# Kernel optimization log

Hardware: AMD Instinct MI355X
Metric: run time of the kernel (lower is better)

Reference implementation:

```python
import jax, jax.numpy as jnp
import numpy as np

N = 50000   # nodes
E = 800000  # edges (avg degree 16)
F_IN, F_HID, F_OUT = 4, 64, 1


def setup_inputs() -> dict:
    key = jax.random.key(0)
    k1, k2, k3, k4 = jax.random.split(key, 4)
    x = jax.random.normal(k1, (N, F_IN), dtype=jnp.float32)
    edge_index = jax.random.randint(k2, (2, E), 0, N, dtype=jnp.int64)
    W1 = jax.random.normal(k3, (F_IN, F_HID), dtype=jnp.float32) * (1.0 / np.sqrt(F_IN))
    b1 = jnp.zeros((F_HID,), dtype=jnp.float32)
    W2 = jax.random.normal(k4, (F_HID, F_OUT), dtype=jnp.float32) * (1.0 / np.sqrt(F_HID))
    b2 = jnp.zeros((F_OUT,), dtype=jnp.float32)
    return {"x": x, "edge_index": edge_index, "W1": W1, "b1": b1, "W2": W2, "b2": b2}


def _gcn_conv(h, W, b, src, dst, norm, n_nodes):
    # h: [N, F_in] -> linear -> gather src -> scale by norm -> scatter-add at dst
    m = (h @ W)[src] * norm[:, None]          # [E+N, F_out]
    out = jax.ops.segment_sum(m, dst, num_segments=n_nodes)
    return out + b


def reference(x, edge_index, W1, b1, W2, b2):
    n = x.shape[0]
    loops = jnp.arange(n, dtype=edge_index.dtype)
    src = jnp.concatenate([edge_index[0], loops])  # add self loops (PyG default)
    dst = jnp.concatenate([edge_index[1], loops])
    # symmetric normalization: deg computed at target (col) as in PyG gcn_norm
    deg = jax.ops.segment_sum(jnp.ones_like(dst, dtype=x.dtype), dst, num_segments=n)
    dis = jnp.where(deg > 0, deg ** -0.5, 0.0)
    norm = dis[src] * dis[dst]                      # [E+N]

    h = jax.nn.relu(_gcn_conv(x, W1, b1, src, dst, norm, n))
    # F.dropout with training=False (inference) is identity
    out = _gcn_conv(h, W2, b2, src, dst, norm, n)
    return jax.nn.sigmoid(out)                      # [N, 1]
```

## Files before the change

kernel.cpp:

```cpp
#include <hip/hip_runtime.h>
#include <hip/hip_fp16.h>


#define FH 64
#define NPB 256
#define MAXBK 512
#define CHB 2048
#define BCAP 8192

__global__ void k_bkt_fill(const int* __restrict__ src, const int* __restrict__ dst,
                           int* __restrict__ bcnt, unsigned int* __restrict__ ebuf,
                           int E, int nbk) {
    __shared__ int h[MAXBK];
    __shared__ int resv[MAXBK];
    int t = threadIdx.x;
    for (int i = t; i < nbk; i += 256) h[i] = 0;
    __syncthreads();
    int base = blockIdx.x * CHB;
    int end = min(base + CHB, E);
    for (int e = base + t; e < end; e += 256)
        atomicAdd(&h[dst[e] >> 8], 1);
    __syncthreads();
    for (int i = t; i < nbk; i += 256) {
        int c = h[i];
        resv[i] = c ? atomicAdd(&bcnt[i], c) : 0;
        h[i] = 0;
    }
    __syncthreads();
    for (int e = base + t; e < end; e += 256) {
        int d = dst[e];
        int b = d >> 8;
        int idx = resv[b] + atomicAdd(&h[b], 1);
        if (idx < BCAP)
            ebuf[(size_t)b * BCAP + idx] = ((unsigned int)d << 16) | (unsigned int)src[e];
    }
}

__global__ void k_bkt_finish(const unsigned int* __restrict__ ebuf,
                             const int* __restrict__ bcnt,
                             int* __restrict__ rowptr, float* __restrict__ dis,
                             unsigned short* __restrict__ csr, int N) {
    __shared__ int sc[NPB];
    __shared__ int f[NPB];
    __shared__ int sbase;
    int b = blockIdx.x, t = threadIdx.x;
    int s = 0;
    for (int i = t; i < b; i += 256) s += bcnt[i];
    sc[t] = s;
    __syncthreads();
    for (int off = 128; off; off >>= 1) {
        if (t < off) sc[t] += sc[t + off];
        __syncthreads();
    }
    if (t == 0) sbase = sc[0];
    __syncthreads();
    int ebase = sbase;
    int cnt = min(bcnt[b], BCAP);
    const unsigned int* eb = ebuf + (size_t)b * BCAP;
    f[t] = 0;
    __syncthreads();
    for (int j = t; j < cnt; j += 256)
        atomicAdd(&f[(eb[j] >> 16) & (NPB - 1)], 1);
    __syncthreads();
    int myc = f[t];
    sc[t] = myc;
    __syncthreads();
    for (int off = 1; off < NPB; off <<= 1) {
        int add = (t >= off) ? sc[t - off] : 0;
        __syncthreads();
        sc[t] += add;
        __syncthreads();
    }
    int ex = ebase + sc[t] - myc;
    int node = b * NPB + t;
    if (node < N) {
        rowptr[node] = ex;
        dis[node] = rsqrtf((float)(myc + 1));
    }
    if (node == N - 1) rowptr[N] = ex + myc;
    __syncthreads();
    f[t] = ex;
    __syncthreads();
    for (int j = t; j < cnt; j += 256) {
        unsigned int pe = eb[j];
        int p = atomicAdd(&f[(pe >> 16) & (NPB - 1)], 1);
        csr[p] = (unsigned short)(pe & 0xffffu);
    }
}

__global__ void k_lin1(const float* __restrict__ x, const float* __restrict__ W1,
                       const float* __restrict__ dis, __half* __restrict__ g, int n) {
    __shared__ float sW[4 * FH];
    int t = threadIdx.x;
    sW[t] = W1[t];
    __syncthreads();
    int node = blockIdx.x * 4 + (t >> 6);
    int f = t & 63;
    if (node < n) {
        float4 xv = *reinterpret_cast<const float4*>(x + (size_t)node * 4);
        float v = xv.x * sW[f] + xv.y * sW[FH + f] + xv.z * sW[2 * FH + f] + xv.w * sW[3 * FH + f];
        g[(size_t)node * FH + f] = __float2half_rn(v * dis[node]);
    }
}

__global__ void k_layer1(const int* __restrict__ rowptr, const unsigned short* __restrict__ csr,
                         const __half* __restrict__ g, const float* __restrict__ dis,
                         const float* __restrict__ b1, const float* __restrict__ W2,
                         float* __restrict__ q, int n) {
    int t = threadIdx.x;
    int node = blockIdx.x * 4 + (t >> 6);
    int f = t & 63;
    if (node >= n) return;
    int rs = rowptr[node], re = rowptr[node + 1];
    float acc = __half2float(g[(size_t)node * FH + f]);
    int j = rs;
    for (; j + 3 < re; j += 4) {
        int s0 = csr[j], s1 = csr[j + 1], s2 = csr[j + 2], s3 = csr[j + 3];
        acc += __half2float(g[(size_t)s0 * FH + f]);
        acc += __half2float(g[(size_t)s1 * FH + f]);
        acc += __half2float(g[(size_t)s2 * FH + f]);
        acc += __half2float(g[(size_t)s3 * FH + f]);
    }
    for (; j < re; ++j) acc += __half2float(g[(size_t)csr[j] * FH + f]);
    float dn = dis[node];
    float h = fmaxf(dn * acc + b1[f], 0.0f);
    float v = h * W2[f];
    #pragma unroll
    for (int off = 32; off; off >>= 1) v += __shfl_xor(v, off, 64);
    if (f == 0) q[node] = v * dn;
}

__global__ void k_layer2(const int* __restrict__ rowptr, const unsigned short* __restrict__ csr,
                         const float* __restrict__ q, const float* __restrict__ dis,
                         const float* __restrict__ b2, float* __restrict__ out, int n) {
    int i = blockIdx.x * blockDim.x + threadIdx.x;
    if (i >= n) return;
    int rs = rowptr[i], re = rowptr[i + 1];
    float acc = q[i];
    for (int j = rs; j < re; ++j) acc += q[csr[j]];
    float v = dis[i] * acc + b2[0];
    out[i] = 1.0f / (1.0f + __expf(-v));
}

extern "C" void kernel_launch(void* const* d_in, const int* in_sizes, int n_in,
                              void* d_out, int out_size, void* d_ws, size_t ws_size,
                              hipStream_t stream) {
    const float* x   = (const float*)d_in[0];
    const int*   ei  = (const int*)d_in[1];
    const float* W1  = (const float*)d_in[2];
    const float* b1  = (const float*)d_in[3];
    const float* W2  = (const float*)d_in[4];
    const float* b2  = (const float*)d_in[5];
    float* out = (float*)d_out;

    int N = in_sizes[0] / 4;
    int E = in_sizes[1] / 2;
    const int* src = ei;
    const int* dst = ei + E;
    int nbk = (N + NPB - 1) / NPB;
    int nbe = (E + CHB - 1) / CHB;

    char* ws = (char*)d_ws;
    size_t off = 0;
    auto alloc = [&](size_t bytes) {
        void* p = ws + off;
        off = (off + bytes + 255) & ~(size_t)255;
        return p;
    };
    int*            rowptr = (int*)alloc((size_t)(N + 1) * 4);
    float*          dis    = (float*)alloc((size_t)N * 4);
    unsigned short* csr    = (unsigned short*)alloc((size_t)E * 2);
    __half*         g      = (__half*)alloc((size_t)N * FH * 2);
    float*          q      = (float*)alloc((size_t)N * 4);
    int*            bcnt   = (int*)alloc((size_t)MAXBK * 4);
    unsigned int*   ebuf   = (unsigned int*)alloc((size_t)nbk * BCAP * 4);
    (void)ws_size;

    hipMemsetAsync(bcnt, 0, (size_t)MAXBK * 4, stream);

    k_bkt_fill<<<nbe, 256, 0, stream>>>(src, dst, bcnt, ebuf, E, nbk);
    k_bkt_finish<<<nbk, 256, 0, stream>>>(ebuf, bcnt, rowptr, dis, csr, N);

    k_lin1<<<(N + 3) / 4, 256, 0, stream>>>(x, W1, dis, g, N);
    k_layer1<<<(N + 3) / 4, 256, 0, stream>>>(rowptr, csr, g, dis, b1, W2, q, N);
    k_layer2<<<(N + 255) / 256, 256, 0, stream>>>(rowptr, csr, q, dis, b2, out, N);
}
```

Measured before the change: 151.3 us.

## Fuse all GCN stages into one cooperative persistent kernel with grid syncs

Replaces the five separate kernel launches with a single cooperative kernel that runs the bucket fill, CSR finish, linear layer, layer-1 aggregation and layer-2 aggregation in sequence, separated by grid-wide barriers. The linear transform no longer depends on the degree normalization, so it is folded into the bucket-fill phase, and the per-source normalization is applied during aggregation instead. The aim is to cut launch and inter-kernel gap overhead. In exchange the aggregation does an extra gather of dis per edge, the grid is fixed at 1024 blocks, and the grid.sync barriers add their own cost.

```diff
diff --git a/kernel.cpp b/kernel.cpp
--- a/kernel.cpp
+++ b/kernel.cpp
@@ -1,5 +1,8 @@
 #include <hip/hip_runtime.h>
 #include <hip/hip_fp16.h>
+#include <hip/hip_cooperative_groups.h>
+
+namespace cg = cooperative_groups;
 
 
 #define FH 64
@@ -7,139 +10,155 @@
 #define MAXBK 512
 #define CHB 2048
 #define BCAP 8192
-
-__global__ void k_bkt_fill(const int* __restrict__ src, const int* __restrict__ dst,
-                           int* __restrict__ bcnt, unsigned int* __restrict__ ebuf,
-                           int E, int nbk) {
+#define GRID_BLKS 1024
+
+struct Params {
+    const int* src; const int* dst;
+    const float* x; const float* W1; const float* b1; const float* W2; const float* b2;
+    float* out;
+    int* rowptr; float* dis; unsigned short* csr; __half* g; float* q;
+    int* bcnt; unsigned int* ebuf;
+    int N, E, nbk, nbe, npass;
+};
+
+__global__ void __launch_bounds__(256) k_mega(Params p) {
+    cg::grid_group grid = cg::this_grid();
+    const int t = threadIdx.x;
+    const int bid = blockIdx.x;
+    const int nb = gridDim.x;
+
     __shared__ int h[MAXBK];
     __shared__ int resv[MAXBK];
-    int t = threadIdx.x;
-    for (int i = t; i < nbk; i += 256) h[i] = 0;
+    __shared__ int sc[NPB];
+    __shared__ int ff[NPB];
+    __shared__ float sW[4 * FH];
+    __shared__ int sbase;
+
+    sW[t] = p.W1[t];
     __syncthreads();
-    int base = blockIdx.x * CHB;
-    int end = min(base + CHB, E);
-    for (int e = base + t; e < end; e += 256)
-        atomicAdd(&h[dst[e] >> 8], 1);
-    __syncthreads();
-    for (int i = t; i < nbk; i += 256) {
-        int c = h[i];
-        resv[i] = c ? atomicAdd(&bcnt[i], c) : 0;
-        h[i] = 0;
-    }
-    __syncthreads();
-    for (int e = base + t; e < end; e += 256) {
-        int d = dst[e];
-        int b = d >> 8;
-        int idx = resv[b] + atomicAdd(&h[b], 1);
-        if (idx < BCAP)
-            ebuf[(size_t)b * BCAP + idx] = ((unsigned int)d << 16) | (unsigned int)src[e];
-    }
-}
-
-__global__ void k_bkt_finish(const unsigned int* __restrict__ ebuf,
-                             const int* __restrict__ bcnt,
-                             int* __restrict__ rowptr, float* __restrict__ dis,
-                             unsigned short* __restrict__ csr, int N) {
-    __shared__ int sc[NPB];
-    __shared__ int f[NPB];
-    __shared__ int sbase;
-    int b = blockIdx.x, t = threadIdx.x;
-    int s = 0;
-    for (int i = t; i < b; i += 256) s += bcnt[i];
-    sc[t] = s;
-    __syncthreads();
-    for (int off = 128; off; off >>= 1) {
-        if (t < off) sc[t] += sc[t + off];
-        __syncthreads();
-    }
-    if (t == 0) sbase = sc[0];
-    __syncthreads();
-    int ebase = sbase;
-    int cnt = min(bcnt[b], BCAP);
-    const unsigned int* eb = ebuf + (size_t)b * BCAP;
-    f[t] = 0;
-    __syncthreads();
-    for (int j = t; j < cnt; j += 256)
-        atomicAdd(&f[(eb[j] >> 16) & (NPB - 1)], 1);
-    __syncthreads();
-    int myc = f[t];
-    sc[t] = myc;
-    __syncthreads();
-    for (int off = 1; off < NPB; off <<= 1) {
-        int add = (t >= off) ? sc[t - off] : 0;
-        __syncthreads();
-        sc[t] += add;
-        __syncthreads();
-    }
-    int ex = ebase + sc[t] - myc;
-    int node = b * NPB + t;
-    if (node < N) {
-        rowptr[node] = ex;
-        dis[node] = rsqrtf((float)(myc + 1));
-    }
-    if (node == N - 1) rowptr[N] = ex + myc;
-    __syncthreads();
-    f[t] = ex;
-    __syncthreads();
-    for (int j = t; j < cnt; j += 256) {
-        unsigned int pe = eb[j];
-        int p = atomicAdd(&f[(pe >> 16) & (NPB - 1)], 1);
-        csr[p] = (unsigned short)(pe & 0xffffu);
-    }
-}
-
-__global__ void k_lin1(const float* __restrict__ x, const float* __restrict__ W1,
-                       const float* __restrict__ dis, __half* __restrict__ g, int n) {
-    __shared__ float sW[4 * FH];
-    int t = threadIdx.x;
-    sW[t] = W1[t];
-    __syncthreads();
-    int node = blockIdx.x * 4 + (t >> 6);
-    int f = t & 63;
-    if (node < n) {
-        float4 xv = *reinterpret_cast<const float4*>(x + (size_t)node * 4);
-        float v = xv.x * sW[f] + xv.y * sW[FH + f] + xv.z * sW[2 * FH + f] + xv.w * sW[3 * FH + f];
-        g[(size_t)node * FH + f] = __float2half_rn(v * dis[node]);
-    }
-}
-
-__global__ void k_layer1(const int* __restrict__ rowptr, const unsigned short* __restrict__ csr,
-                         const __half* __restrict__ g, const float* __restrict__ dis,
-                         const float* __restrict__ b1, const float* __restrict__ W2,
-                         float* __restrict__ q, int n) {
-    int t = threadIdx.x;
-    int node = blockIdx.x * 4 + (t >> 6);
-    int f = t & 63;
-    if (node >= n) return;
-    int rs = rowptr[node], re = rowptr[node + 1];
-    float acc = __half2float(g[(size_t)node * FH + f]);
-    int j = rs;
-    for (; j + 3 < re; j += 4) {
-        int s0 = csr[j], s1 = csr[j + 1], s2 = csr[j + 2], s3 = csr[j + 3];
-        acc += __half2float(g[(size_t)s0 * FH + f]);
-        acc += __half2float(g[(size_t)s1 * FH + f]);
-        acc += __half2float(g[(size_t)s2 * FH + f]);
-        acc += __half2float(g[(size_t)s3 * FH + f]);
-    }
-    for (; j < re; ++j) acc += __half2float(g[(size_t)csr[j] * FH + f]);
-    float dn = dis[node];
-    float h = fmaxf(dn * acc + b1[f], 0.0f);
-    float v = h * W2[f];
-    #pragma unroll
-    for (int off = 32; off; off >>= 1) v += __shfl_xor(v, off, 64);
-    if (f == 0) q[node] = v * dn;
-}
-
-__global__ void k_layer2(const int* __restrict__ rowptr, const unsigned short* __restrict__ csr,
-                         const float* __restrict__ q, const float* __restrict__ dis,
-                         const float* __restrict__ b2, float* __restrict__ out, int n) {
-    int i = blockIdx.x * blockDim.x + threadIdx.x;
-    if (i >= n) return;
-    int rs = rowptr[i], re = rowptr[i + 1];
-    float acc = q[i];
-    for (int j = rs; j < re; ++j) acc += q[csr[j]];
-    float v = dis[i] * acc + b2[0];
-    out[i] = 1.0f / (1.0f + __expf(-v));
+
+    for (int c = bid; c < p.nbe; c += nb) {
+        for (int i = t; i < p.nbk; i += 256) h[i] = 0;
+        __syncthreads();
+        int base = c * CHB, end = min(base + CHB, p.E);
+        for (int e = base + t; e < end; e += 256)
+            atomicAdd(&h[p.dst[e] >> 8], 1);
+        __syncthreads();
+        for (int i = t; i < p.nbk; i += 256) {
+            int cc = h[i];
+            resv[i] = cc ? atomicAdd(&p.bcnt[i], cc) : 0;
+            h[i] = 0;
+        }
+        __syncthreads();
+        for (int e = base + t; e < end; e += 256) {
+            int d = p.dst[e];
+            int b = d >> 8;
+            int idx = resv[b] + atomicAdd(&h[b], 1);
+            if (idx < BCAP)
+                p.ebuf[(size_t)b * BCAP + idx] = ((unsigned)d << 16) | (unsigned)p.src[e];
+        }
+        __syncthreads();
+    }
+
+    for (int pass = bid; pass < p.npass; pass += nb) {
+        int node = pass * 4 + (t >> 6), f = t & 63;
+        if (node < p.N) {
+            float4 xv = *reinterpret_cast<const float4*>(p.x + (size_t)node * 4);
+            float v = xv.x * sW[f] + xv.y * sW[FH + f] + xv.z * sW[2 * FH + f] + xv.w * sW[3 * FH + f];
+            p.g[(size_t)node * FH + f] = __float2half_rn(v);
+        }
+    }
+
+    grid.sync();
+
+    for (int b = bid; b < p.nbk; b += nb) {
+        int s = 0;
+        for (int i = t; i < b; i += 256) s += p.bcnt[i];
+        sc[t] = s;
+        __syncthreads();
+        for (int off = 128; off; off >>= 1) {
+            if (t < off) sc[t] += sc[t + off];
+            __syncthreads();
+        }
+        if (t == 0) sbase = sc[0];
+        __syncthreads();
+        int ebase = sbase;
+        int cnt = min(p.bcnt[b], BCAP);
+        const unsigned int* eb = p.ebuf + (size_t)b * BCAP;
+        ff[t] = 0;
+        __syncthreads();
+        for (int j = t; j < cnt; j += 256)
+            atomicAdd(&ff[(eb[j] >> 16) & (NPB - 1)], 1);
+        __syncthreads();
+        int myc = ff[t];
+        sc[t] = myc;
+        __syncthreads();
+        for (int off = 1; off < NPB; off <<= 1) {
+            int add = (t >= off) ? sc[t - off] : 0;
+            __syncthreads();
+            sc[t] += add;
+            __syncthreads();
+        }
+        int ex = ebase + sc[t] - myc;
+        int node = b * NPB + t;
+        if (node < p.N) {
+            p.rowptr[node] = ex;
+            p.dis[node] = rsqrtf((float)(myc + 1));
+        }
+        if (node == p.N - 1) p.rowptr[p.N] = ex + myc;
+        __syncthreads();
+        ff[t] = ex;
+        __syncthreads();
+        for (int j = t; j < cnt; j += 256) {
+            unsigned int pe = eb[j];
+            int pos = atomicAdd(&ff[(pe >> 16) & (NPB - 1)], 1);
+            p.csr[pos] = (unsigned short)(pe & 0xffffu);
+        }
+        __syncthreads();
+    }
+
+    grid.sync();
+
+    {
+        int f = t & 63;
+        int w = (bid << 2) + (t >> 6);
+        int nw = nb << 2;
+        for (int node = w; node < p.N; node += nw) {
+            int rs = p.rowptr[node], re = p.rowptr[node + 1];
+            float dn = p.dis[node];
+            float acc = dn * __half2float(p.g[(size_t)node * FH + f]);
+            int j = rs;
+            for (; j + 3 < re; j += 4) {
+                int s0 = p.csr[j], s1 = p.csr[j + 1], s2 = p.csr[j + 2], s3 = p.csr[j + 3];
+                acc += p.dis[s0] * __half2float(p.g[(size_t)s0 * FH + f]);
+                acc += p.dis[s1] * __half2float(p.g[(size_t)s1 * FH + f]);
+                acc += p.dis[s2] * __half2float(p.g[(size_t)s2 * FH + f]);
+                acc += p.dis[s3] * __half2float(p.g[(size_t)s3 * FH + f]);
+            }
+            for (; j < re; ++j) {
+                int s0 = p.csr[j];
+                acc += p.dis[s0] * __half2float(p.g[(size_t)s0 * FH + f]);
+            }
+            float hh = fmaxf(dn * acc + p.b1[f], 0.0f);
+            float v = hh * p.W2[f];
+            #pragma unroll
+            for (int off = 32; off; off >>= 1) v += __shfl_xor(v, off, 64);
+            if (f == 0) p.q[node] = v * dn;
+        }
+    }
+
+    grid.sync();
+
+    for (int i = bid * 256 + t; i < p.N; i += nb * 256) {
+        int rs = p.rowptr[i], re = p.rowptr[i + 1];
+        float acc = p.q[i];
+        int j = rs;
+        for (; j + 3 < re; j += 4)
+            acc += p.q[p.csr[j]] + p.q[p.csr[j + 1]] + p.q[p.csr[j + 2]] + p.q[p.csr[j + 3]];
+        for (; j < re; ++j) acc += p.q[p.csr[j]];
+        float v = p.dis[i] * acc + p.b2[0];
+        p.out[i] = 1.0f / (1.0f + __expf(-v));
+    }
 }
 
 extern "C" void kernel_launch(void* const* d_in, const int* in_sizes, int n_in,
@@ -178,10 +197,10 @@
 
     hipMemsetAsync(bcnt, 0, (size_t)MAXBK * 4, stream);
 
-    k_bkt_fill<<<nbe, 256, 0, stream>>>(src, dst, bcnt, ebuf, E, nbk);
-    k_bkt_finish<<<nbk, 256, 0, stream>>>(ebuf, bcnt, rowptr, dis, csr, N);
-
-    k_lin1<<<(N + 3) / 4, 256, 0, stream>>>(x, W1, dis, g, N);
-    k_layer1<<<(N + 3) / 4, 256, 0, stream>>>(rowptr, csr, g, dis, b1, W2, q, N);
-    k_layer2<<<(N + 255) / 256, 256, 0, stream>>>(rowptr, csr, q, dis, b2, out, N);
+    Params p{src, dst, x, W1, b1, W2, b2, out,
+             rowptr, dis, csr, g, q, bcnt, ebuf,
+             N, E, nbk, nbe, (N + 3) / 4};
+    void* args[] = {&p};
+    hipLaunchCooperativeKernel((void*)k_mega, dim3(GRID_BLKS), dim3(256),
+                               args, 0, stream);
 }
```

New measurement: 561.0 us. +270.9%, slower.

## Fuse first linear layer into bucket-fill kernel, apply source norm in gather

Applied to the files above, without the earlier changes.

The x@W1 projection no longer depends on the degree normalization. It now runs in extra blocks of the bucket-fill kernel, removing one kernel launch and the dependency on k_bkt_finish. To make that possible, the per-source dis scaling moves into the layer-1 gather, which now loads dis[src] for every edge. Layer 2's neighbor loop is also unrolled by four. The cost is an extra scattered dis load per edge in the aggregation kernel.

```diff
diff --git a/kernel.cpp b/kernel.cpp
--- a/kernel.cpp
+++ b/kernel.cpp
@@ -7,32 +7,52 @@
 #define MAXBK 512
 #define CHB 2048
 #define BCAP 8192
+#define LIN1_BLKS 2048
 
-__global__ void k_bkt_fill(const int* __restrict__ src, const int* __restrict__ dst,
-                           int* __restrict__ bcnt, unsigned int* __restrict__ ebuf,
-                           int E, int nbk) {
-    __shared__ int h[MAXBK];
-    __shared__ int resv[MAXBK];
+__global__ void k_fill_lin1(const int* __restrict__ src, const int* __restrict__ dst,
+                            int* __restrict__ bcnt, unsigned int* __restrict__ ebuf,
+                            const float* __restrict__ x, const float* __restrict__ W1,
+                            __half* __restrict__ g,
+                            int E, int nbk, int nbe, int N) {
     int t = threadIdx.x;
-    for (int i = t; i < nbk; i += 256) h[i] = 0;
-    __syncthreads();
-    int base = blockIdx.x * CHB;
-    int end = min(base + CHB, E);
-    for (int e = base + t; e < end; e += 256)
-        atomicAdd(&h[dst[e] >> 8], 1);
-    __syncthreads();
-    for (int i = t; i < nbk; i += 256) {
-        int c = h[i];
-        resv[i] = c ? atomicAdd(&bcnt[i], c) : 0;
-        h[i] = 0;
-    }
-    __syncthreads();
-    for (int e = base + t; e < end; e += 256) {
-        int d = dst[e];
-        int b = d >> 8;
-        int idx = resv[b] + atomicAdd(&h[b], 1);
-        if (idx < BCAP)
-            ebuf[(size_t)b * BCAP + idx] = ((unsigned int)d << 16) | (unsigned int)src[e];
+    if ((int)blockIdx.x < nbe) {
+        __shared__ int h[MAXBK];
+        __shared__ int resv[MAXBK];
+        for (int i = t; i < nbk; i += 256) h[i] = 0;
+        __syncthreads();
+        int base = blockIdx.x * CHB;
+        int end = min(base + CHB, E);
+        for (int e = base + t; e < end; e += 256)
+            atomicAdd(&h[dst[e] >> 8], 1);
+        __syncthreads();
+        for (int i = t; i < nbk; i += 256) {
+            int c = h[i];
+            resv[i] = c ? atomicAdd(&bcnt[i], c) : 0;
+            h[i] = 0;
+        }
+        __syncthreads();
+        for (int e = base + t; e < end; e += 256) {
+            int d = dst[e];
+            int b = d >> 8;
+            int idx = resv[b] + atomicAdd(&h[b], 1);
+            if (idx < BCAP)
+                ebuf[(size_t)b * BCAP + idx] = ((unsigned)d << 16) | (unsigned)src[e];
+        }
+    } else {
+        __shared__ float sW[4 * FH];
+        sW[t] = W1[t];
+        __syncthreads();
+        int pass0 = (int)blockIdx.x - nbe;
+        int npass = (N + 3) / 4;
+        int f = t & 63;
+        for (int pass = pass0; pass < npass; pass += LIN1_BLKS) {
+            int node = pass * 4 + (t >> 6);
+            if (node < N) {
+                float4 xv = *reinterpret_cast<const float4*>(x + (size_t)node * 4);
+                float v = xv.x * sW[f] + xv.y * sW[FH + f] + xv.z * sW[2 * FH + f] + xv.w * sW[3 * FH + f];
+                g[(size_t)node * FH + f] = __float2half_rn(v);
+            }
+        }
     }
 }
 
@@ -88,21 +108,6 @@
     }
 }
 
-__global__ void k_lin1(const float* __restrict__ x, const float* __restrict__ W1,
-                       const float* __restrict__ dis, __half* __restrict__ g, int n) {
-    __shared__ float sW[4 * FH];
-    int t = threadIdx.x;
-    sW[t] = W1[t];
-    __syncthreads();
-    int node = blockIdx.x * 4 + (t >> 6);
-    int f = t & 63;
-    if (node < n) {
-        float4 xv = *reinterpret_cast<const float4*>(x + (size_t)node * 4);
-        float v = xv.x * sW[f] + xv.y * sW[FH + f] + xv.z * sW[2 * FH + f] + xv.w * sW[3 * FH + f];
-        g[(size_t)node * FH + f] = __float2half_rn(v * dis[node]);
-    }
-}
-
 __global__ void k_layer1(const int* __restrict__ rowptr, const unsigned short* __restrict__ csr,
                          const __half* __restrict__ g, const float* __restrict__ dis,
                          const float* __restrict__ b1, const float* __restrict__ W2,
@@ -112,17 +117,20 @@
     int f = t & 63;
     if (node >= n) return;
     int rs = rowptr[node], re = rowptr[node + 1];
-    float acc = __half2float(g[(size_t)node * FH + f]);
+    float dn = dis[node];
+    float acc = dn * __half2float(g[(size_t)node * FH + f]);
     int j = rs;
     for (; j + 3 < re; j += 4) {
         int s0 = csr[j], s1 = csr[j + 1], s2 = csr[j + 2], s3 = csr[j + 3];
-        acc += __half2float(g[(size_t)s0 * FH + f]);
-        acc += __half2float(g[(size_t)s1 * FH + f]);
-        acc += __half2float(g[(size_t)s2 * FH + f]);
-        acc += __half2float(g[(size_t)s3 * FH + f]);
+        acc += dis[s0] * __half2float(g[(size_t)s0 * FH + f]);
+        acc += dis[s1] * __half2float(g[(size_t)s1 * FH + f]);
+        acc += dis[s2] * __half2float(g[(size_t)s2 * FH + f]);
+        acc += dis[s3] * __half2float(g[(size_t)s3 * FH + f]);
     }
-    for (; j < re; ++j) acc += __half2float(g[(size_t)csr[j] * FH + f]);
-    float dn = dis[node];
+    for (; j < re; ++j) {
+        int s0 = csr[j];
+        acc += dis[s0] * __half2float(g[(size_t)s0 * FH + f]);
+    }
     float h = fmaxf(dn * acc + b1[f], 0.0f);
     float v = h * W2[f];
     #pragma unroll
@@ -137,7 +145,10 @@
     if (i >= n) return;
     int rs = rowptr[i], re = rowptr[i + 1];
     float acc = q[i];
-    for (int j = rs; j < re; ++j) acc += q[csr[j]];
+    int j = rs;
+    for (; j + 3 < re; j += 4)
+        acc += q[csr[j]] + q[csr[j + 1]] + q[csr[j + 2]] + q[csr[j + 3]];
+    for (; j < re; ++j) acc += q[csr[j]];
     float v = dis[i] * acc + b2[0];
     out[i] = 1.0f / (1.0f + __expf(-v));
 }
@@ -178,10 +189,9 @@
 
     hipMemsetAsync(bcnt, 0, (size_t)MAXBK * 4, stream);
 
-    k_bkt_fill<<<nbe, 256, 0, stream>>>(src, dst, bcnt, ebuf, E, nbk);
+    k_fill_lin1<<<nbe + LIN1_BLKS, 256, 0, stream>>>(src, dst, bcnt, ebuf,
+                                                     x, W1, g, E, nbk, nbe, N);
     k_bkt_finish<<<nbk, 256, 0, stream>>>(ebuf, bcnt, rowptr, dis, csr, N);
-
-    k_lin1<<<(N + 3) / 4, 256, 0, stream>>>(x, W1, dis, g, N);
     k_layer1<<<(N + 3) / 4, 256, 0, stream>>>(rowptr, csr, g, dis, b1, W2, q, N);
     k_layer2<<<(N + 255) / 256, 256, 0, stream>>>(rowptr, csr, q, dis, b2, out, N);
 }
```

Result: faster. 140.7 us (-7.0%).
